# Kernel tuning notes

Hardware: AMD Instinct MI355X
Metric: run time of the kernel (lower is better)

Reference implementation:

```python
import math
import jax, jax.numpy as jnp
import numpy as np

B, T, D, NH = 4, 2048, 1024, 16
HS = D // NH
N_BUCKETS = 32
MAX_DIST = 128


def _relative_position_bucket(rp):
    # bidirectional T5 bucketing, n_buckets=32, max_distance=128
    nb = N_BUCKETS // 2  # 16
    buckets = (rp > 0).astype(jnp.int32) * nb
    rp = jnp.abs(rp)
    max_exact = nb // 2  # 8
    is_small = rp < max_exact
    me = max_exact - 1   # 7
    nbm = nb - 1         # 15
    rp_safe = jnp.maximum(rp, 1).astype(jnp.float32)
    rp_large = me + (jnp.log(rp_safe / me) / math.log(MAX_DIST / me) * (nbm - me)).astype(jnp.int32)
    rp_large = jnp.minimum(rp_large, nbm)
    buckets = buckets + jnp.where(is_small, rp, rp_large)
    return buckets


def compute_bias(rel_emb, qT, kT):
    ctx = jnp.arange(qT, dtype=jnp.int32)[:, None]
    mem = jnp.arange(kT, dtype=jnp.int32)[None, :]
    bucket = _relative_position_bucket(mem - ctx)  # [qT, kT]
    values = rel_emb[bucket]                        # [qT, kT, NH]
    return jnp.transpose(values, (2, 0, 1))[None]   # [1, NH, qT, kT]


def setup_inputs() -> dict:
    key = jax.random.key(0)
    ks = jax.random.split(key, 6)
    s = 0.02
    return {
        "queries": jax.random.normal(ks[0], (B, T, D), jnp.float32),
        "Wq": jax.random.normal(ks[1], (D, D), jnp.float32) * s,
        "Wk": jax.random.normal(ks[2], (D, D), jnp.float32) * s,
        "Wv": jax.random.normal(ks[3], (D, D), jnp.float32) * s,
        "Wo": jax.random.normal(ks[4], (D, D), jnp.float32) * s,
        "rel_emb": jax.random.normal(ks[5], (N_BUCKETS, NH), jnp.float32) * s,
    }


def reference(queries, Wq, Wk, Wv, Wo, rel_emb):
    b, t, d = queries.shape
    def split_heads(x):
        return jnp.transpose(x.reshape(b, t, NH, HS), (0, 2, 1, 3))  # [B, nh, T, hs]
    q = split_heads(queries @ Wq.T)
    k = split_heads(queries @ Wk.T)
    v = split_heads(queries @ Wv.T)
    att = jnp.einsum('bhqd,bhkd->bhqk', q, k) * (1.0 / math.sqrt(HS))
    att = att + compute_bias(rel_emb, t, t)
    att = jax.nn.softmax(att, axis=-1)
    o = jnp.einsum('bhqk,bhkd->bhqd', att, v)
    o = jnp.transpose(o, (0, 2, 1, 3)).reshape(b, t, d)
    return o @ Wo.T
```

## Files before the change

### kernel.cpp

```cpp
#include <hip/hip_runtime.h>
#include <math.h>

#define T_SEQ 2048
#define D_MODEL 1024
#define NHEADS 16
#define HSZ 64
#define BATCH 4

typedef __bf16 bf16x8 __attribute__((ext_vector_type(8)));
typedef __bf16 bf16x4 __attribute__((ext_vector_type(4)));
typedef short short4v __attribute__((ext_vector_type(4)));
typedef float f32x4 __attribute__((ext_vector_type(4)));
typedef float f32x16 __attribute__((ext_vector_type(16)));

__device__ __forceinline__ unsigned short f2bf(float f) {
    unsigned int u = __builtin_bit_cast(unsigned int, f);
    u += 0x7fff + ((u >> 16) & 1);
    return (unsigned short)(u >> 16);
}

__device__ __forceinline__ unsigned int pk2bf(float a, float b) {
#if __has_builtin(__builtin_amdgcn_cvt_pk_bf16_f32)
    typedef __bf16 bf16x2_t __attribute__((ext_vector_type(2)));
    bf16x2_t v = __builtin_amdgcn_cvt_pk_bf16_f32(a, b);
    return __builtin_bit_cast(unsigned int, v);
#else
    return (unsigned int)f2bf(a) | ((unsigned int)f2bf(b) << 16);
#endif
}

__device__ __forceinline__ float fexp2(float x) {
#if __has_builtin(__builtin_amdgcn_exp2f)
    return __builtin_amdgcn_exp2f(x);
#else
    return __builtin_exp2f(x);
#endif
}

__device__ __forceinline__ void pl32swap(unsigned int& a, unsigned int& b) {
#if __has_builtin(__builtin_amdgcn_permlane32_swap)
    auto r = __builtin_amdgcn_permlane32_swap((int)a, (int)b, false, false);
    a = (unsigned int)r[0];
    b = (unsigned int)r[1];
#else
    unsigned int sa = (unsigned int)__shfl_xor((int)a, 32);
    unsigned int sb = (unsigned int)__shfl_xor((int)b, 32);
    const int hi = (int)((threadIdx.x & 63) >> 5);
    unsigned int na = hi ? sb : a;
    unsigned int nb = hi ? b : sa;
    a = na; b = nb;
#endif
}

__device__ __forceinline__ void gld_lds16(const void* g, void* lds) {
    __builtin_amdgcn_global_load_lds(
        (const __attribute__((address_space(1))) unsigned int*)g,
        (__attribute__((address_space(3))) unsigned int*)lds, 16, 0, 0);
}

__device__ __forceinline__ bf16x8 ld8(const unsigned short* p) {
    return *(const bf16x8*)p;
}

__device__ __forceinline__ float t5_bias(int delta, int h, const float* __restrict__ rel) {
    int bucket = delta > 0 ? 16 : 0;
    int arp = delta < 0 ? -delta : delta;
    if (arp < 8) {
        bucket += arp;
    } else {
        float f = logf((float)arp / 7.0f) * (8.0f / logf(128.0f / 7.0f));
        int rl = 7 + (int)f;
        bucket += rl < 15 ? rl : 15;
    }
    return rel[bucket * NHEADS + h] * 1.4426950408889634f;
}

__global__ void prep(const float* __restrict__ x,
                     const float* __restrict__ w0, const float* __restrict__ w1,
                     const float* __restrict__ w2, const float* __restrict__ w3,
                     unsigned short* __restrict__ Xbf,
                     unsigned short* __restrict__ Wbf) {
    int bid = blockIdx.x;
    int tid = threadIdx.x;
    if (bid < 8192) {
        int i = bid * 256 + tid;
        float4 v = ((const float4*)x)[i];
        ushort4 o;
        o.x = f2bf(v.x); o.y = f2bf(v.y); o.z = f2bf(v.z); o.w = f2bf(v.w);
        ((ushort4*)Xbf)[i] = o;
    } else {
        int wsel = (bid - 8192) >> 10;
        const float* srcs[4] = {w0, w1, w2, w3};
        int i = ((bid - 8192) & 1023) * 256 + tid;
        float4 v = ((const float4*)srcs[wsel])[i];
        ushort4 o;
        o.x = f2bf(v.x); o.y = f2bf(v.y); o.z = f2bf(v.z); o.w = f2bf(v.w);
        ((ushort4*)(Wbf + (size_t)wsel * 1048576))[i] = o;
    }
}

template<int MODE>
__global__ __launch_bounds__(256, 2) void gemm_bt(
    const unsigned short* __restrict__ A,
    const unsigned short* __restrict__ Bw,
    void* __restrict__ out)
{
    constexpr int K = 1024;
    __shared__ __align__(16) char smem[65536];

    const int tid  = threadIdx.x;
    const int wave = tid >> 6;
    const int lane = tid & 63;
    const int quad = lane >> 4;
    const int l16  = lane & 15;
    const int wm   = wave >> 1;
    const int wn   = wave & 1;

    constexpr int NWGX = (MODE == 4) ? 24 : 8;
    const int orig = blockIdx.x + blockIdx.y * NWGX;
    constexpr int CPX = (NWGX * 64) / 8;
    const int swz  = (orig & 7) * CPX + (orig >> 3);
    const int bn   = swz % NWGX;
    const int bm   = swz / NWGX;

    const int r_in = lane >> 3;
    const int lc   = (lane & 7) ^ r_in;

    f32x4 acc[4][4];
    #pragma unroll
    for (int m = 0; m < 4; ++m)
        #pragma unroll
        for (int n = 0; n < 4; ++n)
            acc[m][n] = f32x4{0.f, 0.f, 0.f, 0.f};

    const long a_row0 = (long)bm * 128;
    const long b_row0 = (long)bn * 128;

    {
        const int k0 = lc * 8;
        unsigned short* As_ = (unsigned short*)smem;
        unsigned short* Bs_ = (unsigned short*)(smem + 16384);
        #pragma unroll
        for (int c = 0; c < 4; ++c) {
            int cc = wave * 4 + c;
            int r  = cc * 8 + r_in;
            gld_lds16(A  + (a_row0 + r) * K + k0, &As_[cc * 512]);
            gld_lds16(Bw + (b_row0 + r) * K + k0, &Bs_[cc * 512]);
        }
    }

    for (int kt = 0; kt < K / 64; ++kt) {
        const int cur = kt & 1;
        __syncthreads();

        if (kt + 1 < K / 64) {
            const int k0 = (kt + 1) * 64 + lc * 8;
            unsigned short* As_ = (unsigned short*)(smem + (cur ^ 1) * 32768);
            unsigned short* Bs_ = (unsigned short*)(smem + (cur ^ 1) * 32768 + 16384);
            #pragma unroll
            for (int c = 0; c < 4; ++c) {
                int cc = wave * 4 + c;
                int r  = cc * 8 + r_in;
                gld_lds16(A  + (a_row0 + r) * K + k0, &As_[cc * 512]);
                gld_lds16(Bw + (b_row0 + r) * K + k0, &Bs_[cc * 512]);
            }
        }

        unsigned short* As = (unsigned short*)(smem + cur * 32768);
        unsigned short* Bs = (unsigned short*)(smem + cur * 32768 + 16384);

        bf16x8 af[4][2], bf[4][2];
        #pragma unroll
        for (int m = 0; m < 4; ++m)
            #pragma unroll
            for (int ks = 0; ks < 2; ++ks) {
                int r  = wm * 64 + m * 16 + l16;
                int pc = (ks * 4 + quad) ^ (r & 7);
                af[m][ks] = ld8(&As[r * 64 + pc * 8]);
            }
        #pragma unroll
        for (int n = 0; n < 4; ++n)
            #pragma unroll
            for (int ks = 0; ks < 2; ++ks) {
                int r  = wn * 64 + n * 16 + l16;
                int pc = (ks * 4 + quad) ^ (r & 7);
                bf[n][ks] = ld8(&Bs[r * 64 + pc * 8]);
            }
        #pragma unroll
        for (int ks = 0; ks < 2; ++ks)
            #pragma unroll
            for (int m = 0; m < 4; ++m)
                #pragma unroll
                for (int n = 0; n < 4; ++n)
                    acc[m][n] = __builtin_amdgcn_mfma_f32_16x16x32_bf16(
                        af[m][ks], bf[n][ks], acc[m][n], 0, 0, 0);
    }

    const int which = (MODE == 4) ? (bn >> 3) : 0;
    if (MODE == 3) {
        float* O = (float*)out;
        #pragma unroll
        for (int m = 0; m < 4; ++m) {
            int row = bm * 128 + wm * 64 + m * 16 + quad * 4;
            #pragma unroll
            for (int n = 0; n < 4; ++n) {
                int col = bn * 128 + wn * 64 + n * 16 + l16;
                #pragma unroll
                for (int r = 0; r < 4; ++r)
                    O[(long)(row + r) * 1024 + col] = acc[m][n][r];
            }
        }
    } else if (which == 2) {
        unsigned short* O = (unsigned short*)out + (size_t)2 * 8388608;
        #pragma unroll
        for (int m = 0; m < 4; ++m) {
            int row = bm * 128 + wm * 64 + m * 16 + quad * 4;
            int b = row >> 11, t = row & 2047;
            #pragma unroll
            for (int n = 0; n < 4; ++n) {
                int cl = (bn * 128 + wn * 64 + n * 16 + l16) & 1023;
                int h = cl >> 6, hs = cl & 63;
                ushort4 pk;
                pk.x = f2bf(acc[m][n][0]); pk.y = f2bf(acc[m][n][1]);
                pk.z = f2bf(acc[m][n][2]); pk.w = f2bf(acc[m][n][3]);
                *(ushort4*)&O[(long)((b * 16 + h) * 64 + hs) * 2048 + t] = pk;
            }
        }
    } else {
        __syncthreads();
        unsigned short* Ew = (unsigned short*)smem + wave * 4608;
        const float qs = (which == 0) ? 0.125f * 1.4426950408889634f : 1.0f;
        #pragma unroll
        for (int m = 0; m < 4; ++m)
            #pragma unroll
            for (int n = 0; n < 4; ++n)
                #pragma unroll
                for (int r = 0; r < 4; ++r)
                    Ew[(m * 16 + quad * 4 + r) * 72 + n * 16 + l16] =
                        f2bf(acc[m][n][r] * qs);
        asm volatile("s_waitcnt lgkmcnt(0)" ::: "memory");

        const int cl0 = (bn * 128 + wn * 64) & 1023;
        const int h   = cl0 >> 6;
        const int gr0 = bm * 128 + wm * 64;
        const int b   = gr0 >> 11, t0 = gr0 & 2047;
        unsigned short* O = (unsigned short*)out + (size_t)which * 8388608
                          + ((size_t)(b * 16 + h) * 2048 + t0) * 64;
        #pragma unroll
        for (int rr = 0; rr < 8; ++rr) {
            int row   = rr * 8 + (lane >> 3);
            int chunk = lane & 7;
            uint4 v = *(const uint4*)&Ew[row * 72 + chunk * 8];
            *(uint4*)&O[(size_t)row * 64 + chunk * 8] = v;
        }
    }
}

__global__ __launch_bounds__(256, 4) void attn(
    const unsigned short* __restrict__ Q,
    const unsigned short* __restrict__ Kb,
    const unsigned short* __restrict__ Vt,
    const float* __restrict__ rel,
    unsigned short* __restrict__ AO)
{
    __shared__ __align__(16) char smem[33824];
    unsigned short* KsB = (unsigned short*)smem;
    unsigned short* VsB = (unsigned short*)(smem + 16384);
    float*          Bb  = (float*)(smem + 32768);

    const int tid  = threadIdx.x;
    const int wave = tid >> 6;
    const int lane = tid & 63;
    const int l31  = lane & 31;
    const int h5   = lane >> 5;

    const int bh = blockIdx.y;
    const int b  = bh >> 4, h = bh & 15;
    const int q0 = blockIdx.x * 128;

    const unsigned short* Qg = Q  + (long)bh * T_SEQ * HSZ;
    const unsigned short* Kg = Kb + (long)bh * T_SEQ * HSZ;
    const unsigned short* Vg = Vt + (long)bh * HSZ * T_SEQ;

    const int r_in = lane >> 3;
    const int lc   = (lane & 7) ^ r_in;

    {
        #pragma unroll
        for (int c = 0; c < 2; ++c) {
            int cc = wave * 2 + c;
            int r  = cc * 8 + r_in;
            gld_lds16(Kg + (long)r * 64 + lc * 8, &KsB[cc * 512]);
            gld_lds16(Vg + (long)r * T_SEQ + lc * 8, &VsB[cc * 512]);
        }
    }

    for (int i = tid; i < 263; i += 256)
        Bb[i] = t5_bias(i - 131, h, rel);

    const int qrow_lane = q0 + wave * 32 + l31;
    bf16x8 qf[4];
    #pragma unroll
    for (int hsc = 0; hsc < 4; ++hsc)
        qf[hsc] = ld8(&Qg[(long)qrow_lane * 64 + hsc * 16 + h5 * 8]);

    f32x16 o0 = {0.f,0.f,0.f,0.f,0.f,0.f,0.f,0.f,0.f,0.f,0.f,0.f,0.f,0.f,0.f,0.f};
    f32x16 o1 = o0;
    float li = 0.0f;

    const float cneg = rel[15 * NHEADS + h] * 1.4426950408889634f;
    const float cpos = rel[31 * NHEADS + h] * 1.4426950408889634f;

    for (int kt = 0; kt < T_SEQ / 64; ++kt) {
        const int cur = kt & 1;
        __syncthreads();

        if (kt + 1 < T_SEQ / 64) {
            unsigned short* Kn = KsB + (cur ^ 1) * 4096;
            unsigned short* Vn = VsB + (cur ^ 1) * 4096;
            #pragma unroll
            for (int c = 0; c < 2; ++c) {
                int cc = wave * 2 + c;
                int r  = cc * 8 + r_in;
                gld_lds16(Kg + (long)((kt + 1) * 64 + r) * 64 + lc * 8, &Kn[cc * 512]);
                gld_lds16(Vg + (long)r * T_SEQ + (kt + 1) * 64 + lc * 8, &Vn[cc * 512]);
            }
        }

        const unsigned short* Ks = KsB + cur * 4096;
        const unsigned short* Vs = VsB + cur * 4096;

        const int lo = kt * 64 - q0 - 127;
        const int hi = kt * 64 + 63 - q0;
        const bool outband = (lo >= 128) || (hi <= -128);
        const float cb = (lo >= 128) ? cpos : cneg;

        #pragma unroll
        for (int tt = 0; tt < 2; ++tt) {
            const int rk = tt * 32 + l31;
            bf16x8 af[4];
            #pragma unroll
            for (int hsc = 0; hsc < 4; ++hsc)
                af[hsc] = ld8(&Ks[rk * 64 + (((hsc << 1) | h5) ^ (rk & 7)) * 8]);

            float bb[16];
            if (outband) {
                #pragma unroll
                for (int e = 0; e < 16; ++e) bb[e] = cb;
            } else {
                const int ibase = kt * 64 + tt * 32 + h5 * 4 + 131 - qrow_lane;
                #pragma unroll
                for (int g = 0; g < 4; ++g) {
                    int i0 = ibase + g * 8;
                    i0 = i0 < 0 ? 0 : (i0 > 259 ? 259 : i0);
                    #pragma unroll
                    for (int r = 0; r < 4; ++r) bb[g * 4 + r] = Bb[i0 + r];
                }
            }

            f32x16 s = {0.f,0.f,0.f,0.f,0.f,0.f,0.f,0.f,
                        0.f,0.f,0.f,0.f,0.f,0.f,0.f,0.f};
            __builtin_amdgcn_s_setprio(1);
            #pragma unroll
            for (int hsc = 0; hsc < 4; ++hsc)
                s = __builtin_amdgcn_mfma_f32_32x32x16_bf16(af[hsc], qf[hsc], s, 0, 0, 0);
            __builtin_amdgcn_s_setprio(0);

            float p[16];
            #pragma unroll
            for (int e = 0; e < 16; ++e) p[e] = fexp2(s[e] + bb[e]);
            {
                float t0 = (p[0]  + p[1])  + (p[2]  + p[3]);
                float t1 = (p[4]  + p[5])  + (p[6]  + p[7]);
                float t2 = (p[8]  + p[9])  + (p[10] + p[11]);
                float t3 = (p[12] + p[13]) + (p[14] + p[15]);
                li += (t0 + t1) + (t2 + t3);
            }

            unsigned int x0 = pk2bf(p[0],  p[1]),  x1 = pk2bf(p[2],  p[3]);
            unsigned int y0 = pk2bf(p[4],  p[5]),  y1 = pk2bf(p[6],  p[7]);
            unsigned int z0 = pk2bf(p[8],  p[9]),  z1 = pk2bf(p[10], p[11]);
            unsigned int u0 = pk2bf(p[12], p[13]), u1 = pk2bf(p[14], p[15]);
            pl32swap(x0, y0); pl32swap(x1, y1);
            pl32swap(z0, u0); pl32swap(z1, u1);
            uint4 pw0 = {x0, x1, y0, y1};
            uint4 pw1 = {z0, z1, u0, u1};
            bf16x8 pf[2] = {__builtin_bit_cast(bf16x8, pw0),
                            __builtin_bit_cast(bf16x8, pw1)};

            #pragma unroll
            for (int c = 0; c < 2; ++c) {
                const int tc = tt * 2 + c;
                const int rv0 = l31;
                const int rv1 = 32 + l31;
                bf16x8 vf0 = ld8(&Vs[rv0 * 64 + (((tc << 1) | h5) ^ (rv0 & 7)) * 8]);
                bf16x8 vf1 = ld8(&Vs[rv1 * 64 + (((tc << 1) | h5) ^ (rv1 & 7)) * 8]);
                __builtin_amdgcn_s_setprio(1);
                o0 = __builtin_amdgcn_mfma_f32_32x32x16_bf16(pf[c], vf0, o0, 0, 0, 0);
                o1 = __builtin_amdgcn_mfma_f32_32x32x16_bf16(pf[c], vf1, o1, 0, 0, 0);
                __builtin_amdgcn_s_setprio(0);
            }
        }
    }

    li += __shfl_xor(li, 32);
    const float inv = 1.0f / li;

    #pragma unroll
    for (int g = 0; g < 4; ++g) {
        #pragma unroll
        for (int r = 0; r < 4; ++r) {
            const int ql = g * 8 + h5 * 4 + r;
            const float iv = __shfl(inv, ql);
            const int qrow = q0 + wave * 32 + ql;
            unsigned short* dst =
                &AO[(long)(b * T_SEQ + qrow) * D_MODEL + h * 64 + l31];
            dst[0]  = f2bf(o0[g * 4 + r] * iv);
            dst[32] = f2bf(o1[g * 4 + r] * iv);
        }
    }
}

extern "C" void kernel_launch(void* const* d_in, const int* in_sizes, int n_in,
                              void* d_out, int out_size, void* d_ws, size_t ws_size,
                              hipStream_t stream) {
    const float* x   = (const float*)d_in[0];
    const float* wq  = (const float*)d_in[1];
    const float* wk  = (const float*)d_in[2];
    const float* wv  = (const float*)d_in[3];
    const float* wo  = (const float*)d_in[4];
    const float* rel = (const float*)d_in[5];

    char* ws = (char*)d_ws;
    unsigned short* Xbf = (unsigned short*)(ws);
    unsigned short* Wbf = (unsigned short*)(ws + (16l << 20));
    unsigned short* Qb  = (unsigned short*)(ws + (24l << 20));

    prep<<<12288, 256, 0, stream>>>(x, wq, wk, wv, wo, Xbf, Wbf);

    gemm_bt<4><<<dim3(24, 64), 256, 0, stream>>>(Xbf, Wbf, Qb);

    unsigned short* Kbf = Qb + 8388608;
    unsigned short* Vtb = Qb + 16777216;
    unsigned short* AO  = Xbf;
    attn<<<dim3(16, 64), 256, 0, stream>>>(Qb, Kbf, Vtb, rel, AO);

    gemm_bt<3><<<dim3(8, 64), 256, 0, stream>>>(AO, Wbf + 3 * 1048576, d_out);
}
```

Before: 270.4 us.

## Enlarge GEMM block tile to 256x256 with 512-thread workgroups

Both projection GEMMs now use 256x256 output tiles computed by 8 waves, each owning a 128x64 sub-tile, with 128KB of double-buffered LDS. The inner loop is reordered to load B fragments once per k-step and stream A fragments per row block, which lowers register pressure. The goal is more operand reuse per global and LDS load. The cost is that the grid shrinks to 384 and 128 workgroups, so the output GEMM cannot fill all CUs, and the large LDS footprint limits occupancy to one block per CU.

```diff
diff --git a/kernel.cpp b/kernel.cpp
--- a/kernel.cpp
+++ b/kernel.cpp
@@ -100,25 +100,26 @@
 }
 
 template<int MODE>
-__global__ __launch_bounds__(256, 2) void gemm_bt(
+__global__ __launch_bounds__(512, 2) void gemm_bt(
     const unsigned short* __restrict__ A,
     const unsigned short* __restrict__ Bw,
     void* __restrict__ out)
 {
     constexpr int K = 1024;
-    __shared__ __align__(16) char smem[65536];
+    __shared__ __align__(16) char smem[131072];
 
     const int tid  = threadIdx.x;
     const int wave = tid >> 6;
     const int lane = tid & 63;
     const int quad = lane >> 4;
     const int l16  = lane & 15;
-    const int wm   = wave >> 1;
-    const int wn   = wave & 1;
-
-    constexpr int NWGX = (MODE == 4) ? 24 : 8;
+    const int wm   = wave >> 2;
+    const int wn   = wave & 3;
+
+    constexpr int NWGX  = (MODE == 4) ? 12 : 4;
+    constexpr int TOTAL = NWGX * 32;
+    constexpr int CPX   = TOTAL / 8;
     const int orig = blockIdx.x + blockIdx.y * NWGX;
-    constexpr int CPX = (NWGX * 64) / 8;
     const int swz  = (orig & 7) * CPX + (orig >> 3);
     const int bn   = swz % NWGX;
     const int bm   = swz / NWGX;
@@ -126,20 +127,20 @@
     const int r_in = lane >> 3;
     const int lc   = (lane & 7) ^ r_in;
 
-    f32x4 acc[4][4];
+    f32x4 acc[8][4];
     #pragma unroll
-    for (int m = 0; m < 4; ++m)
+    for (int m = 0; m < 8; ++m)
         #pragma unroll
         for (int n = 0; n < 4; ++n)
             acc[m][n] = f32x4{0.f, 0.f, 0.f, 0.f};
 
-    const long a_row0 = (long)bm * 128;
-    const long b_row0 = (long)bn * 128;
+    const long a_row0 = (long)bm * 256;
+    const long b_row0 = (long)bn * 256;
 
     {
         const int k0 = lc * 8;
         unsigned short* As_ = (unsigned short*)smem;
-        unsigned short* Bs_ = (unsigned short*)(smem + 16384);
+        unsigned short* Bs_ = (unsigned short*)(smem + 32768);
         #pragma unroll
         for (int c = 0; c < 4; ++c) {
             int cc = wave * 4 + c;
@@ -155,8 +156,8 @@
 
         if (kt + 1 < K / 64) {
             const int k0 = (kt + 1) * 64 + lc * 8;
-            unsigned short* As_ = (unsigned short*)(smem + (cur ^ 1) * 32768);
-            unsigned short* Bs_ = (unsigned short*)(smem + (cur ^ 1) * 32768 + 16384);
+            unsigned short* As_ = (unsigned short*)(smem + (cur ^ 1) * 65536);
+            unsigned short* Bs_ = (unsigned short*)(smem + (cur ^ 1) * 65536 + 32768);
             #pragma unroll
             for (int c = 0; c < 4; ++c) {
                 int cc = wave * 4 + c;
@@ -166,45 +167,40 @@
             }
         }
 
-        unsigned short* As = (unsigned short*)(smem + cur * 32768);
-        unsigned short* Bs = (unsigned short*)(smem + cur * 32768 + 16384);
-
-        bf16x8 af[4][2], bf[4][2];
-        #pragma unroll
-        for (int m = 0; m < 4; ++m)
-            #pragma unroll
-            for (int ks = 0; ks < 2; ++ks) {
-                int r  = wm * 64 + m * 16 + l16;
-                int pc = (ks * 4 + quad) ^ (r & 7);
-                af[m][ks] = ld8(&As[r * 64 + pc * 8]);
-            }
-        #pragma unroll
-        for (int n = 0; n < 4; ++n)
-            #pragma unroll
-            for (int ks = 0; ks < 2; ++ks) {
+        unsigned short* As = (unsigned short*)(smem + cur * 65536);
+        unsigned short* Bs = (unsigned short*)(smem + cur * 65536 + 32768);
+
+        #pragma unroll
+        for (int ks = 0; ks < 2; ++ks) {
+            bf16x8 bf[4];
+            #pragma unroll
+            for (int n = 0; n < 4; ++n) {
                 int r  = wn * 64 + n * 16 + l16;
                 int pc = (ks * 4 + quad) ^ (r & 7);
-                bf[n][ks] = ld8(&Bs[r * 64 + pc * 8]);
-            }
-        #pragma unroll
-        for (int ks = 0; ks < 2; ++ks)
-            #pragma unroll
-            for (int m = 0; m < 4; ++m)
+                bf[n] = ld8(&Bs[r * 64 + pc * 8]);
+            }
+            #pragma unroll
+            for (int m = 0; m < 8; ++m) {
+                int r  = wm * 128 + m * 16 + l16;
+                int pc = (ks * 4 + quad) ^ (r & 7);
+                bf16x8 af = ld8(&As[r * 64 + pc * 8]);
                 #pragma unroll
                 for (int n = 0; n < 4; ++n)
                     acc[m][n] = __builtin_amdgcn_mfma_f32_16x16x32_bf16(
-                        af[m][ks], bf[n][ks], acc[m][n], 0, 0, 0);
-    }
-
-    const int which = (MODE == 4) ? (bn >> 3) : 0;
+                        af, bf[n], acc[m][n], 0, 0, 0);
+            }
+        }
+    }
+
+    const int which = (MODE == 4) ? (bn >> 2) : 0;
     if (MODE == 3) {
         float* O = (float*)out;
         #pragma unroll
-        for (int m = 0; m < 4; ++m) {
-            int row = bm * 128 + wm * 64 + m * 16 + quad * 4;
+        for (int m = 0; m < 8; ++m) {
+            int row = bm * 256 + wm * 128 + m * 16 + quad * 4;
             #pragma unroll
             for (int n = 0; n < 4; ++n) {
-                int col = bn * 128 + wn * 64 + n * 16 + l16;
+                int col = bn * 256 + wn * 64 + n * 16 + l16;
                 #pragma unroll
                 for (int r = 0; r < 4; ++r)
                     O[(long)(row + r) * 1024 + col] = acc[m][n][r];
@@ -213,12 +209,12 @@
     } else if (which == 2) {
         unsigned short* O = (unsigned short*)out + (size_t)2 * 8388608;
         #pragma unroll
-        for (int m = 0; m < 4; ++m) {
-            int row = bm * 128 + wm * 64 + m * 16 + quad * 4;
+        for (int m = 0; m < 8; ++m) {
+            int row = bm * 256 + wm * 128 + m * 16 + quad * 4;
             int b = row >> 11, t = row & 2047;
             #pragma unroll
             for (int n = 0; n < 4; ++n) {
-                int cl = (bn * 128 + wn * 64 + n * 16 + l16) & 1023;
+                int cl = (bn * 256 + wn * 64 + n * 16 + l16) & 1023;
                 int h = cl >> 6, hs = cl & 63;
                 ushort4 pk;
                 pk.x = f2bf(acc[m][n][0]); pk.y = f2bf(acc[m][n][1]);
@@ -230,28 +226,31 @@
         __syncthreads();
         unsigned short* Ew = (unsigned short*)smem + wave * 4608;
         const float qs = (which == 0) ? 0.125f * 1.4426950408889634f : 1.0f;
-        #pragma unroll
-        for (int m = 0; m < 4; ++m)
-            #pragma unroll
-            for (int n = 0; n < 4; ++n)
+        const int cl0 = (bn * 256 + wn * 64) & 1023;
+        const int h   = cl0 >> 6;
+        #pragma unroll
+        for (int mh = 0; mh < 2; ++mh) {
+            #pragma unroll
+            for (int mm = 0; mm < 4; ++mm)
                 #pragma unroll
-                for (int r = 0; r < 4; ++r)
-                    Ew[(m * 16 + quad * 4 + r) * 72 + n * 16 + l16] =
-                        f2bf(acc[m][n][r] * qs);
-        asm volatile("s_waitcnt lgkmcnt(0)" ::: "memory");
-
-        const int cl0 = (bn * 128 + wn * 64) & 1023;
-        const int h   = cl0 >> 6;
-        const int gr0 = bm * 128 + wm * 64;
-        const int b   = gr0 >> 11, t0 = gr0 & 2047;
-        unsigned short* O = (unsigned short*)out + (size_t)which * 8388608
-                          + ((size_t)(b * 16 + h) * 2048 + t0) * 64;
-        #pragma unroll
-        for (int rr = 0; rr < 8; ++rr) {
-            int row   = rr * 8 + (lane >> 3);
-            int chunk = lane & 7;
-            uint4 v = *(const uint4*)&Ew[row * 72 + chunk * 8];
-            *(uint4*)&O[(size_t)row * 64 + chunk * 8] = v;
+                for (int n = 0; n < 4; ++n)
+                    #pragma unroll
+                    for (int r = 0; r < 4; ++r)
+                        Ew[(mm * 16 + quad * 4 + r) * 72 + n * 16 + l16] =
+                            f2bf(acc[mh * 4 + mm][n][r] * qs);
+            asm volatile("s_waitcnt lgkmcnt(0)" ::: "memory");
+
+            const int gr0 = bm * 256 + wm * 128 + mh * 64;
+            const int b   = gr0 >> 11, t0 = gr0 & 2047;
+            unsigned short* O = (unsigned short*)out + (size_t)which * 8388608
+                              + ((size_t)(b * 16 + h) * 2048 + t0) * 64;
+            #pragma unroll
+            for (int rr = 0; rr < 8; ++rr) {
+                int row   = rr * 8 + (lane >> 3);
+                int chunk = lane & 7;
+                uint4 v = *(const uint4*)&Ew[row * 72 + chunk * 8];
+                *(uint4*)&O[(size_t)row * 64 + chunk * 8] = v;
+            }
         }
     }
 }
@@ -438,12 +437,12 @@
 
     prep<<<12288, 256, 0, stream>>>(x, wq, wk, wv, wo, Xbf, Wbf);
 
-    gemm_bt<4><<<dim3(24, 64), 256, 0, stream>>>(Xbf, Wbf, Qb);
+    gemm_bt<4><<<dim3(12, 32), 512, 0, stream>>>(Xbf, Wbf, Qb);
 
     unsigned short* Kbf = Qb + 8388608;
     unsigned short* Vtb = Qb + 16777216;
     unsigned short* AO  = Xbf;
     attn<<<dim3(16, 64), 256, 0, stream>>>(Qb, Kbf, Vtb, rel, AO);
 
-    gemm_bt<3><<<dim3(8, 64), 256, 0, stream>>>(AO, Wbf + 3 * 1048576, d_out);
-}
+    gemm_bt<3><<<dim3(4, 32), 512, 0, stream>>>(AO, Wbf + 3 * 1048576, d_out);
+}
```

After: 299.6 us. 10.8% more time.
